# Optimization experiments

Measured on AMD Instinct MI355X. Metric: run time of the kernel, lower is better.

The kernel has to match this reference:

```python
import jax, jax.numpy as jnp
import numpy as np

EPS = 1e-5  # BatchNorm3d default eps


def conv1x1(x, w, b):
    # x: (b, cin, t, h, w); w: (cout, cin); b: (cout,)
    return jnp.einsum('bcthw,oc->bothw', x, w) + b[None, :, None, None, None]


def batchnorm(x):
    # BatchNorm3d(affine=False), training mode: per-channel batch stats over (B,T,H,W)
    mean = jnp.mean(x, axis=(0, 2, 3, 4), keepdims=True)
    var = jnp.var(x, axis=(0, 2, 3, 4), keepdims=True)
    return (x - mean) * jax.lax.rsqrt(var + EPS)


def setup_inputs() -> dict:
    key = jax.random.key(0)
    ks = jax.random.split(key, 9)
    B, C, T, H, W = 4, 512, 16, 14, 14
    IC = C // 4
    s_in = 1.0 / np.sqrt(C)
    s_up = 1.0 / np.sqrt(IC)
    return {
        'maps':    jax.random.normal(ks[0], (B, C, T, H, W), jnp.float32),
        'w_theta': jax.random.uniform(ks[1], (IC, C), jnp.float32, -s_in, s_in),
        'b_theta': jax.random.uniform(ks[2], (IC,),   jnp.float32, -s_in, s_in),
        'w_phalt': jax.random.uniform(ks[3], (IC, C), jnp.float32, -s_in, s_in),
        'b_phalt': jax.random.uniform(ks[4], (IC,),   jnp.float32, -s_in, s_in),
        'w_glob':  jax.random.uniform(ks[5], (IC, C), jnp.float32, -s_in, s_in),
        'b_glob':  jax.random.uniform(ks[6], (IC,),   jnp.float32, -s_in, s_in),
        'w_up':    jax.random.uniform(ks[7], (C, IC), jnp.float32, -s_up, s_up),
        'b_up':    jax.random.uniform(ks[8], (C,),    jnp.float32, -s_up, s_up),
    }


def reference(maps, w_theta, b_theta, w_phalt, b_phalt, w_glob, b_glob, w_up, b_up):
    b, c, t, h, w = maps.shape
    ic = c // 4
    n = t * h * w

    theta_maps = batchnorm(conv1x1(maps, w_theta, b_theta))   # (b, ic, t, h, w)
    phalt_maps = batchnorm(conv1x1(maps, w_phalt, b_phalt))   # computed but UNUSED (bug in original)
    global_maps = batchnorm(conv1x1(maps, w_glob, b_glob))

    theta_x = theta_maps.reshape(b, ic, n)                    # (b, ic, n)
    # NOTE: original code uses theta_maps for phalt_x (faithful to source bug)
    relation = jnp.einsum('bcn,bcm->bnm', theta_x, theta_x)   # (b, n, n)
    relation_normalize = jax.nn.softmax(relation / n, axis=-1)

    global_x = global_maps.reshape(b, ic, n)                  # (b, ic, n)
    y = jnp.einsum('bnm,bcm->bcn', relation_normalize, global_x)
    y = y.reshape(b, ic, t, h, w)

    out = conv1x1(y, w_up, b_up) + maps
    return out
```

## Files before the change

### kernel.cpp

```cpp
#include <hip/hip_runtime.h>
#include <hip/hip_bf16.h>


typedef __attribute__((ext_vector_type(8))) short bf16x8;
typedef __attribute__((ext_vector_type(4))) float f32x4;
typedef __attribute__((ext_vector_type(4))) short s16x4;
typedef __attribute__((ext_vector_type(2))) unsigned int u32x2;

#define NTOK 3136
#define NELEM 1605632
#define NSPLIT 4

__device__ inline float bf2f(short u) {
    union { unsigned int i; float f; } v;
    v.i = ((unsigned int)(unsigned short)u) << 16;
    return v.f;
}
__device__ inline short f2bf(float x) {
    union { float f; unsigned int i; } v;
    v.f = x;
    unsigned int r = v.i + 0x7FFFu + ((v.i >> 16) & 1u);
    return (short)(r >> 16);
}
__device__ inline unsigned int tbf(float x) {
    union { float f; unsigned int i; } v;
    v.f = x;
    return v.i >> 16;
}
__device__ inline void glds16(const void* g, void* l) {
    __builtin_amdgcn_global_load_lds((const __attribute__((address_space(1))) void*)g,
                                     (__attribute__((address_space(3))) void*)l, 16, 0, 0);
}

__global__ __launch_bounds__(256) void prep_w(const float* __restrict__ wt,
                                              const float* __restrict__ wg,
                                              const float* __restrict__ wup,
                                              short* __restrict__ Wb,
                                              short* __restrict__ wupb)
{
    const int i = blockIdx.x * 256 + threadIdx.x;
    if (i < 131072) {
        const int r = i >> 9;
        const int c = i & 511;
        const float w = (r < 128) ? wt[(size_t)r * 512 + c] : wg[(size_t)(r - 128) * 512 + c];
        Wb[i] = f2bf(w);
    } else {
        const int j = i - 131072;
        wupb[j] = f2bf(wup[j]);
    }
}

__global__ __launch_bounds__(256) void conv_in_f(const float* __restrict__ maps,
                                                 const short* __restrict__ Wb,
                                                 short* __restrict__ Tt,
                                                 short* __restrict__ Gpre,
                                                 float* __restrict__ psum,
                                                 float* __restrict__ psq)
{
    const int nt = blockIdx.x, b = blockIdx.y;
    const int n0 = nt * 32;
    const int t = threadIdx.x;
    const int w = __builtin_amdgcn_readfirstlane(t >> 6);
    const int lane = t & 63;
    const int l15 = lane & 15, lhi = lane >> 4;

    __shared__ short Bt[32][136];

    const float* mp = maps + (size_t)b * 512 * NTOK + n0;
    const int cl = t >> 3;
    const int f4 = t & 7;

    f32x4 acc[4][2];
#pragma unroll
    for (int g = 0; g < 4; g++)
#pragma unroll
        for (int j = 0; j < 2; j++) acc[g][j] = f32x4{0.f, 0.f, 0.f, 0.f};

    f32x4 rg[4];
#pragma unroll
    for (int p = 0; p < 4; p++)
        rg[p] = *(const f32x4*)(mp + (size_t)(p * 32 + cl) * NTOK + f4 * 4);

    for (int kc = 0; kc < 4; kc++) {
        __syncthreads();
#pragma unroll
        for (int p = 0; p < 4; p++) {
            const int cc = p * 32 + cl;
#pragma unroll
            for (int i = 0; i < 4; i++) Bt[f4 * 4 + i][cc] = f2bf(rg[p][i]);
        }
        if (kc < 3) {
#pragma unroll
            for (int p = 0; p < 4; p++)
                rg[p] = *(const f32x4*)(mp + (size_t)((kc + 1) * 128 + p * 32 + cl) * NTOK + f4 * 4);
        }
        __syncthreads();
#pragma unroll
        for (int ks = 0; ks < 4; ks++) {
            bf16x8 af[4], bv[2];
#pragma unroll
            for (int g = 0; g < 4; g++)
                af[g] = *(const bf16x8*)(Wb + (size_t)(w * 64 + g * 16 + l15) * 512 + kc * 128 + ks * 32 + lhi * 8);
#pragma unroll
            for (int j = 0; j < 2; j++)
                bv[j] = *(const bf16x8*)(&Bt[j * 16 + l15][ks * 32 + lhi * 8]);
#pragma unroll
            for (int g = 0; g < 4; g++)
#pragma unroll
                for (int j = 0; j < 2; j++)
                    acc[g][j] = __builtin_amdgcn_mfma_f32_16x16x32_bf16(af[g], bv[j], acc[g][j], 0, 0, 0);
        }
    }

    if (w < 2) {
#pragma unroll
        for (int g = 0; g < 4; g++)
#pragma unroll
            for (int j = 0; j < 2; j++) {
                s16x4 v;
#pragma unroll
                for (int r = 0; r < 4; r++) v[r] = f2bf(acc[g][j][r]);
                *(s16x4*)(Tt + ((size_t)b * NTOK + n0 + j * 16 + l15) * 128 + w * 64 + g * 16 + lhi * 4) = v;
            }
    } else {
#pragma unroll
        for (int g = 0; g < 4; g++)
#pragma unroll
            for (int j = 0; j < 2; j++)
#pragma unroll
                for (int r = 0; r < 4; r++) {
                    const int icg = (w - 2) * 64 + g * 16 + lhi * 4 + r;
                    Gpre[((size_t)b * 128 + icg) * NTOK + n0 + j * 16 + l15] = f2bf(acc[g][j][r]);
                }
    }
#pragma unroll
    for (int g = 0; g < 4; g++)
#pragma unroll
        for (int r = 0; r < 4; r++) {
            float s = acc[g][0][r] + acc[g][1][r];
            float q = acc[g][0][r] * acc[g][0][r] + acc[g][1][r] * acc[g][1][r];
#pragma unroll
            for (int off = 1; off < 16; off <<= 1) {
                s += __shfl_xor(s, off);
                q += __shfl_xor(q, off);
            }
            if (l15 == 0) {
                const int ch = w * 64 + g * 16 + lhi * 4 + r;
                psum[(size_t)ch * 392 + b * 98 + nt] = s;
                psq [(size_t)ch * 392 + b * 98 + nt] = q;
            }
        }
}

__global__ __launch_bounds__(64) void stats_fin(const float* __restrict__ psum,
                                                const float* __restrict__ psq,
                                                float* __restrict__ st)
{
    const int ch = blockIdx.x;
    const int lane = threadIdx.x;
    float s = 0.f, q = 0.f;
    for (int i = lane; i < 392; i += 64) {
        s += psum[(size_t)ch * 392 + i];
        q += psq [(size_t)ch * 392 + i];
    }
#pragma unroll
    for (int off = 32; off; off >>= 1) { s += __shfl_xor(s, off); q += __shfl_xor(q, off); }
    if (lane == 0) {
        const float mean = s / 12544.f;
        const float var = q / 12544.f - mean * mean;
        st[ch] = mean;
        st[256 + ch] = rsqrtf(var + 1e-5f);
    }
}

__global__ __launch_bounds__(256) void attn_k(const short* __restrict__ Tt,
                                              const short* __restrict__ Gpre,
                                              const float* __restrict__ st,
                                              float* __restrict__ Opart,
                                              float* __restrict__ dpart)
{
    constexpr int N = NTOK;
    const int b = blockIdx.y, s = blockIdx.z;
    const int w = __builtin_amdgcn_readfirstlane(threadIdx.x >> 6);
    const int lane = threadIdx.x & 63;
    const int l15 = lane & 15, lhi = lane >> 4;
    const int q0w = blockIdx.x * 128 + w * 32;

    __shared__ __align__(16) short Kl[2][64][128];
    __shared__ __align__(16) short Vl[2][128][64];
    __shared__ __align__(16) short Pl[4][32][64];

    const short* tb = Tt + (size_t)b * N * 128;
    const short* gb = Gpre + (size_t)b * 128 * N;

    bf16x8 qf[2][4];
#pragma unroll
    for (int qs = 0; qs < 2; qs++) {
        int row = q0w + qs * 16 + l15;
        row = row < N ? row : N - 1;
#pragma unroll
        for (int ks = 0; ks < 4; ks++) {
            const bf16x8 v = *(const bf16x8*)(tb + (size_t)row * 128 + ks * 32 + lhi * 8);
            const int c0 = ks * 32 + lhi * 8;
            const f32x4 mA = *(const f32x4*)(st + c0);
            const f32x4 mB = *(const f32x4*)(st + c0 + 4);
            const f32x4 rA = *(const f32x4*)(st + 256 + c0);
            const f32x4 rB = *(const f32x4*)(st + 256 + c0 + 4);
            bf16x8 q;
#pragma unroll
            for (int j = 0; j < 4; j++) q[j] = f2bf((bf2f(v[j]) - mA[j]) * (rA[j] * rA[j]));
#pragma unroll
            for (int j = 0; j < 4; j++) q[4 + j] = f2bf((bf2f(v[4 + j]) - mB[j]) * (rB[j] * rB[j]));
            qf[qs][ks] = q;
        }
    }

    f32x4 acc[2][8];
#pragma unroll
    for (int qs = 0; qs < 2; qs++)
#pragma unroll
        for (int is = 0; is < 8; is++) acc[qs][is] = f32x4{0.f, 0.f, 0.f, 0.f};
    float denom[2] = {0.f, 0.f};
    const float inv_n = 1.0f / (float)N;

    auto STAGE = [&](int bufi, int m0) {
#pragma unroll
        for (int i = 0; i < 4; i++) {
            const int rb = w * 16 + i * 4;
            const int krow = rb + (lane >> 4);
            const int ksw = ((lane & 15) * 16) ^ ((krow & 7) << 4);
            glds16((const char*)tb + (size_t)(m0 + krow) * 256 + ksw, (char*)&Kl[bufi][rb][0]);
        }
#pragma unroll
        for (int i = 0; i < 4; i++) {
            const int rb = w * 32 + i * 8;
            const int vrow = rb + (lane >> 3);
            const int vsw = ((lane & 7) * 16) ^ ((vrow & 7) << 4);
            glds16((const char*)gb + ((size_t)vrow * N + m0) * 2 + vsw, (char*)&Vl[bufi][rb][0]);
        }
    };

    const int nt = (49 - s + NSPLIT - 1) / NSPLIT;
    int mt = s;
    STAGE(0, mt * 64);
    __syncthreads();
    int buf = 0;

    const int fK = (l15 & 7) << 4;

    for (int t = 0; t < nt; ++t) {
        if (t + 1 < nt) STAGE(buf ^ 1, (mt + NSPLIT) * 64);

        f32x4 sv[2][4];
#pragma unroll
        for (int qs = 0; qs < 2; qs++)
#pragma unroll
            for (int ms = 0; ms < 4; ms++) sv[qs][ms] = f32x4{0.f, 0.f, 0.f, 0.f};
#pragma unroll
        for (int ms = 0; ms < 4; ms++) {
            const char* kbase = (const char*)&Kl[buf][ms * 16 + l15][0];
#pragma unroll
            for (int ks = 0; ks < 4; ks++) {
                bf16x8 kf = *(const bf16x8*)(kbase + ((ks * 64 + lhi * 16) ^ fK));
                sv[0][ms] = __builtin_amdgcn_mfma_f32_16x16x32_bf16(kf, qf[0][ks], sv[0][ms], 0, 0, 0);
                sv[1][ms] = __builtin_amdgcn_mfma_f32_16x16x32_bf16(kf, qf[1][ks], sv[1][ms], 0, 0, 0);
            }
        }
#pragma unroll
        for (int qs = 0; qs < 2; qs++) {
            char* pbase = (char*)&Pl[w][qs * 16 + l15][0];
#pragma unroll
            for (int ms = 0; ms < 4; ms++) {
                const float p0 = __expf(sv[qs][ms][0] * inv_n);
                const float p1 = __expf(sv[qs][ms][1] * inv_n);
                const float p2 = __expf(sv[qs][ms][2] * inv_n);
                const float p3 = __expf(sv[qs][ms][3] * inv_n);
                denom[qs] += (p0 + p1) + (p2 + p3);
                u32x2 u;
                u[0] = tbf(p0) | (tbf(p1) << 16);
                u[1] = tbf(p2) | (tbf(p3) << 16);
                *(u32x2*)(pbase + ((ms * 32 + lhi * 8) ^ fK)) = u;
            }
        }
#pragma unroll
        for (int kp = 0; kp < 2; kp++) {
            const int coff = kp * 64 + lhi * 16;
            bf16x8 pa[2];
#pragma unroll
            for (int qs = 0; qs < 2; qs++)
                pa[qs] = *(const bf16x8*)((const char*)&Pl[w][qs * 16 + l15][0] + (coff ^ fK));
#pragma unroll
            for (int is = 0; is < 8; is++) {
                bf16x8 vf = *(const bf16x8*)((const char*)&Vl[buf][is * 16 + l15][0] + (coff ^ fK));
                acc[0][is] = __builtin_amdgcn_mfma_f32_16x16x32_bf16(pa[0], vf, acc[0][is], 0, 0, 0);
                acc[1][is] = __builtin_amdgcn_mfma_f32_16x16x32_bf16(pa[1], vf, acc[1][is], 0, 0, 0);
            }
        }
        __syncthreads();
        buf ^= 1;
        mt += NSPLIT;
    }

#pragma unroll
    for (int qs = 0; qs < 2; qs++) {
        denom[qs] += __shfl_xor(denom[qs], 16);
        denom[qs] += __shfl_xor(denom[qs], 32);
    }

    float* op = Opart + ((size_t)(s * 4 + b)) * N * 128;
#pragma unroll
    for (int qs = 0; qs < 2; qs++)
#pragma unroll
        for (int is = 0; is < 8; is++)
#pragma unroll
            for (int r = 0; r < 4; r++) {
                const int n = q0w + qs * 16 + lhi * 4 + r;
                if (n < N) op[(size_t)n * 128 + is * 16 + l15] = acc[qs][is][r];
            }
    if (lhi == 0) {
#pragma unroll
        for (int qs = 0; qs < 2; qs++) {
            const int n = q0w + qs * 16 + l15;
            if (n < N) dpart[(size_t)(s * 4 + b) * N + n] = denom[qs];
        }
    }
}

__global__ __launch_bounds__(256) void conv_out_f(const float* __restrict__ Opart,
                                                  const float* __restrict__ dpart,
                                                  const float* __restrict__ st,
                                                  const short* __restrict__ wupb,
                                                  const float* __restrict__ bup,
                                                  const float* __restrict__ maps,
                                                  float* __restrict__ out)
{
    const int n0 = blockIdx.x * 32, b = blockIdx.y;
    const int t = threadIdx.x;

    __shared__ float denl[32];
    __shared__ __align__(16) short Yl[32][128];

    if (t < 32) {
        float d = 0.f;
#pragma unroll
        for (int s = 0; s < NSPLIT; s++) d += dpart[(size_t)(s * 4 + b) * NTOK + n0 + t];
        denl[t] = 1.0f / d;
    }
    __syncthreads();

#pragma unroll
    for (int g = 0; g < 2; g++) {
        const int e = t + g * 256;
        const int nl = e >> 4, icg = (e & 15) * 8;
        const float rdn = denl[nl];
        float sum[8] = {0.f, 0.f, 0.f, 0.f, 0.f, 0.f, 0.f, 0.f};
#pragma unroll
        for (int s = 0; s < NSPLIT; s++) {
            const size_t base = ((size_t)(s * 4 + b) * NTOK + n0 + nl) * 128 + icg;
            const f32x4 a = *(const f32x4*)(Opart + base);
            const f32x4 c = *(const f32x4*)(Opart + base + 4);
#pragma unroll
            for (int j = 0; j < 4; j++) { sum[j] += a[j]; sum[4 + j] += c[j]; }
        }
        const f32x4 mA = *(const f32x4*)(st + 128 + icg);
        const f32x4 mB = *(const f32x4*)(st + 128 + icg + 4);
        const f32x4 rA = *(const f32x4*)(st + 384 + icg);
        const f32x4 rB = *(const f32x4*)(st + 384 + icg + 4);
        s16x4 v0, v1;
#pragma unroll
        for (int j = 0; j < 4; j++) v0[j] = f2bf((sum[j] * rdn - mA[j]) * rA[j]);
#pragma unroll
        for (int j = 0; j < 4; j++) v1[j] = f2bf((sum[4 + j] * rdn - mB[j]) * rB[j]);
        char* ybase = (char*)&Yl[nl][0];
        const int sw = (nl & 7) << 4;
        *(s16x4*)(ybase + ((icg * 2) ^ sw)) = v0;
        *(s16x4*)(ybase + (((icg * 2) ^ sw) + 8)) = v1;
    }
    __syncthreads();

    const int wv = __builtin_amdgcn_readfirstlane(t >> 6);
    const int lane = t & 63;
    const int l15 = lane & 15, lhi = lane >> 4;
    const int c0 = wv * 128;
    const int fY = (l15 & 7) << 4;

    f32x4 acc[8][2];
#pragma unroll
    for (int g = 0; g < 8; g++)
#pragma unroll
        for (int j = 0; j < 2; j++) acc[g][j] = f32x4{0.f, 0.f, 0.f, 0.f};

#pragma unroll
    for (int ks = 0; ks < 4; ks++) {
        bf16x8 af[8], bv[2];
#pragma unroll
        for (int g = 0; g < 8; g++)
            af[g] = *(const bf16x8*)(wupb + (size_t)(c0 + g * 16 + l15) * 128 + ks * 32 + lhi * 8);
#pragma unroll
        for (int j = 0; j < 2; j++)
            bv[j] = *(const bf16x8*)((const char*)&Yl[j * 16 + l15][0] + ((ks * 64 + lhi * 16) ^ fY));
#pragma unroll
        for (int g = 0; g < 8; g++)
#pragma unroll
            for (int j = 0; j < 2; j++)
                acc[g][j] = __builtin_amdgcn_mfma_f32_16x16x32_bf16(af[g], bv[j], acc[g][j], 0, 0, 0);
    }
#pragma unroll
    for (int g = 0; g < 8; g++)
#pragma unroll
        for (int j = 0; j < 2; j++)
#pragma unroll
            for (int r = 0; r < 4; r++) {
                const int c = c0 + g * 16 + lhi * 4 + r;
                const int n = n0 + j * 16 + l15;
                const size_t o = ((size_t)b * 512 + c) * NTOK + n;
                out[o] = acc[g][j][r] + bup[c] + maps[o];
            }
}

extern "C" void kernel_launch(void* const* d_in, const int* in_sizes, int n_in,
                              void* d_out, int out_size, void* d_ws, size_t ws_size,
                              hipStream_t stream)
{
    const float* maps    = (const float*)d_in[0];
    const float* w_theta = (const float*)d_in[1];
    const float* w_glob  = (const float*)d_in[5];
    const float* w_up    = (const float*)d_in[7];
    const float* b_up    = (const float*)d_in[8];
    float* out = (float*)d_out;

    short* Tt    = (short*)d_ws;
    short* Gpre  = Tt + NELEM;
    short* Wb    = Gpre + NELEM;
    short* wupb  = Wb + 131072;
    float* st    = (float*)(wupb + 65536);
    float* psum  = st + 512;
    float* psq   = psum + 100352;
    float* dpart = psq + 100352;
    float* Opart = dpart + 50176;

    prep_w    <<<768,             256, 0, stream>>>(w_theta, w_glob, w_up, Wb, wupb);
    conv_in_f <<<dim3(98, 4),     256, 0, stream>>>(maps, Wb, Tt, Gpre, psum, psq);
    stats_fin <<<256,             64,  0, stream>>>(psum, psq, st);
    attn_k    <<<dim3(25, 4, NSPLIT), 256, 0, stream>>>(Tt, Gpre, st, Opart, dpart);
    conv_out_f<<<dim3(98, 4),     256, 0, stream>>>(Opart, dpart, st, wupb, b_up, maps, out);
}
```

Measured before the change: 91.88 us.

## Switch attention to 32x32x16 MFMA and keep P in registers via permlane swap

The attention kernel moves from 16x16x32 to 32x32x16 bf16 MFMA tiles for both QK^T and PV. The softmax probabilities are now packed and rearranged in registers with v_permlane32_swap instead of going through a per-wave LDS buffer, which removes the P LDS round-trip and its shared memory. Launch bounds now request 2 blocks per CU. The larger accumulators raise register pressure, and the new fragment mapping must match the 32x32 MFMA layout to stay correct.

```diff
diff --git a/kernel.cpp b/kernel.cpp
--- a/kernel.cpp
+++ b/kernel.cpp
@@ -4,8 +4,8 @@
 
 typedef __attribute__((ext_vector_type(8))) short bf16x8;
 typedef __attribute__((ext_vector_type(4))) float f32x4;
+typedef __attribute__((ext_vector_type(16))) float f32x16;
 typedef __attribute__((ext_vector_type(4))) short s16x4;
-typedef __attribute__((ext_vector_type(2))) unsigned int u32x2;
 
 #define NTOK 3136
 #define NELEM 1605632
@@ -22,10 +22,13 @@
     unsigned int r = v.i + 0x7FFFu + ((v.i >> 16) & 1u);
     return (short)(r >> 16);
 }
-__device__ inline unsigned int tbf(float x) {
-    union { float f; unsigned int i; } v;
-    v.f = x;
-    return v.i >> 16;
+__device__ inline unsigned pk2(float lo, float hi) {
+    union { float f; unsigned u; } a, b;
+    a.f = lo; b.f = hi;
+    return __builtin_amdgcn_perm(b.u, a.u, 0x07060302u);
+}
+__device__ inline void pl32swap(unsigned &a, unsigned &b) {
+    asm("v_permlane32_swap_b32 %0, %1" : "+v"(a), "+v"(b));
 }
 __device__ inline void glds16(const void* g, void* l) {
     __builtin_amdgcn_global_load_lds((const __attribute__((address_space(1))) void*)g,
@@ -173,35 +176,33 @@
     }
 }
 
-__global__ __launch_bounds__(256) void attn_k(const short* __restrict__ Tt,
-                                              const short* __restrict__ Gpre,
-                                              const float* __restrict__ st,
-                                              float* __restrict__ Opart,
-                                              float* __restrict__ dpart)
+__global__ __launch_bounds__(256, 2) void attn_k(const short* __restrict__ Tt,
+                                                 const short* __restrict__ Gpre,
+                                                 const float* __restrict__ st,
+                                                 float* __restrict__ Opart,
+                                                 float* __restrict__ dpart)
 {
     constexpr int N = NTOK;
     const int b = blockIdx.y, s = blockIdx.z;
     const int w = __builtin_amdgcn_readfirstlane(threadIdx.x >> 6);
     const int lane = threadIdx.x & 63;
-    const int l15 = lane & 15, lhi = lane >> 4;
+    const int l31 = lane & 31, hi = lane >> 5;
     const int q0w = blockIdx.x * 128 + w * 32;
 
     __shared__ __align__(16) short Kl[2][64][128];
     __shared__ __align__(16) short Vl[2][128][64];
-    __shared__ __align__(16) short Pl[4][32][64];
 
     const short* tb = Tt + (size_t)b * N * 128;
     const short* gb = Gpre + (size_t)b * 128 * N;
 
-    bf16x8 qf[2][4];
-#pragma unroll
-    for (int qs = 0; qs < 2; qs++) {
-        int row = q0w + qs * 16 + l15;
-        row = row < N ? row : N - 1;
-#pragma unroll
-        for (int ks = 0; ks < 4; ks++) {
-            const bf16x8 v = *(const bf16x8*)(tb + (size_t)row * 128 + ks * 32 + lhi * 8);
-            const int c0 = ks * 32 + lhi * 8;
+    bf16x8 qf[8];
+    {
+        int row = q0w + l31; row = row < N ? row : N - 1;
+        const short* qp = tb + (size_t)row * 128;
+#pragma unroll
+        for (int ks = 0; ks < 8; ks++) {
+            const int c0 = ks * 16 + hi * 8;
+            const bf16x8 v = *(const bf16x8*)(qp + c0);
             const f32x4 mA = *(const f32x4*)(st + c0);
             const f32x4 mB = *(const f32x4*)(st + c0 + 4);
             const f32x4 rA = *(const f32x4*)(st + 256 + c0);
@@ -211,16 +212,16 @@
             for (int j = 0; j < 4; j++) q[j] = f2bf((bf2f(v[j]) - mA[j]) * (rA[j] * rA[j]));
 #pragma unroll
             for (int j = 0; j < 4; j++) q[4 + j] = f2bf((bf2f(v[4 + j]) - mB[j]) * (rB[j] * rB[j]));
-            qf[qs][ks] = q;
-        }
-    }
-
-    f32x4 acc[2][8];
-#pragma unroll
-    for (int qs = 0; qs < 2; qs++)
-#pragma unroll
-        for (int is = 0; is < 8; is++) acc[qs][is] = f32x4{0.f, 0.f, 0.f, 0.f};
-    float denom[2] = {0.f, 0.f};
+            qf[ks] = q;
+        }
+    }
+
+    f32x16 accv[4];
+#pragma unroll
+    for (int it = 0; it < 4; it++)
+#pragma unroll
+        for (int r = 0; r < 16; r++) accv[it][r] = 0.f;
+    float denom = 0.f;
     const float inv_n = 1.0f / (float)N;
 
     auto STAGE = [&](int bufi, int m0) {
@@ -228,15 +229,15 @@
         for (int i = 0; i < 4; i++) {
             const int rb = w * 16 + i * 4;
             const int krow = rb + (lane >> 4);
-            const int ksw = ((lane & 15) * 16) ^ ((krow & 7) << 4);
-            glds16((const char*)tb + (size_t)(m0 + krow) * 256 + ksw, (char*)&Kl[bufi][rb][0]);
+            const int ls = (lane & 15) ^ (krow & 7);
+            glds16(tb + (size_t)(m0 + krow) * 128 + ls * 8, (void*)&Kl[bufi][rb][0]);
         }
 #pragma unroll
         for (int i = 0; i < 4; i++) {
             const int rb = w * 32 + i * 8;
             const int vrow = rb + (lane >> 3);
-            const int vsw = ((lane & 7) * 16) ^ ((vrow & 7) << 4);
-            glds16((const char*)gb + ((size_t)vrow * N + m0) * 2 + vsw, (char*)&Vl[bufi][rb][0]);
+            const int ls = (lane & 7) ^ (vrow & 7);
+            glds16(gb + (size_t)vrow * N + m0 + ls * 8, (void*)&Vl[bufi][rb][0]);
         }
     };
 
@@ -246,54 +247,50 @@
     __syncthreads();
     int buf = 0;
 
-    const int fK = (l15 & 7) << 4;
+    const int fr = (l31 & 7) << 4;
+
+    auto mkpa = [&](const f32x16 &sv, bf16x8 *dst) {
+        float e[16];
+#pragma unroll
+        for (int r = 0; r < 16; r++) { e[r] = __expf(sv[r] * inv_n); denom += e[r]; }
+        unsigned c0 = pk2(e[0], e[1]),  c1 = pk2(e[2], e[3]);
+        unsigned c2 = pk2(e[4], e[5]),  c3 = pk2(e[6], e[7]);
+        unsigned c4 = pk2(e[8], e[9]),  c5 = pk2(e[10], e[11]);
+        unsigned c6 = pk2(e[12], e[13]), c7 = pk2(e[14], e[15]);
+        pl32swap(c0, c2); pl32swap(c1, c3); pl32swap(c4, c6); pl32swap(c5, c7);
+        union U { unsigned u[4]; bf16x8 v; } f0, f1;
+        f0.u[0] = c0; f0.u[1] = c1; f0.u[2] = c2; f0.u[3] = c3;
+        f1.u[0] = c4; f1.u[1] = c5; f1.u[2] = c6; f1.u[3] = c7;
+        dst[0] = f0.v; dst[1] = f1.v;
+    };
 
     for (int t = 0; t < nt; ++t) {
         if (t + 1 < nt) STAGE(buf ^ 1, (mt + NSPLIT) * 64);
 
-        f32x4 sv[2][4];
-#pragma unroll
-        for (int qs = 0; qs < 2; qs++)
-#pragma unroll
-            for (int ms = 0; ms < 4; ms++) sv[qs][ms] = f32x4{0.f, 0.f, 0.f, 0.f};
-#pragma unroll
-        for (int ms = 0; ms < 4; ms++) {
-            const char* kbase = (const char*)&Kl[buf][ms * 16 + l15][0];
-#pragma unroll
-            for (int ks = 0; ks < 4; ks++) {
-                bf16x8 kf = *(const bf16x8*)(kbase + ((ks * 64 + lhi * 16) ^ fK));
-                sv[0][ms] = __builtin_amdgcn_mfma_f32_16x16x32_bf16(kf, qf[0][ks], sv[0][ms], 0, 0, 0);
-                sv[1][ms] = __builtin_amdgcn_mfma_f32_16x16x32_bf16(kf, qf[1][ks], sv[1][ms], 0, 0, 0);
-            }
-        }
-#pragma unroll
-        for (int qs = 0; qs < 2; qs++) {
-            char* pbase = (char*)&Pl[w][qs * 16 + l15][0];
-#pragma unroll
-            for (int ms = 0; ms < 4; ms++) {
-                const float p0 = __expf(sv[qs][ms][0] * inv_n);
-                const float p1 = __expf(sv[qs][ms][1] * inv_n);
-                const float p2 = __expf(sv[qs][ms][2] * inv_n);
-                const float p3 = __expf(sv[qs][ms][3] * inv_n);
-                denom[qs] += (p0 + p1) + (p2 + p3);
-                u32x2 u;
-                u[0] = tbf(p0) | (tbf(p1) << 16);
-                u[1] = tbf(p2) | (tbf(p3) << 16);
-                *(u32x2*)(pbase + ((ms * 32 + lhi * 8) ^ fK)) = u;
-            }
-        }
-#pragma unroll
-        for (int kp = 0; kp < 2; kp++) {
-            const int coff = kp * 64 + lhi * 16;
-            bf16x8 pa[2];
-#pragma unroll
-            for (int qs = 0; qs < 2; qs++)
-                pa[qs] = *(const bf16x8*)((const char*)&Pl[w][qs * 16 + l15][0] + (coff ^ fK));
-#pragma unroll
-            for (int is = 0; is < 8; is++) {
-                bf16x8 vf = *(const bf16x8*)((const char*)&Vl[buf][is * 16 + l15][0] + (coff ^ fK));
-                acc[0][is] = __builtin_amdgcn_mfma_f32_16x16x32_bf16(pa[0], vf, acc[0][is], 0, 0, 0);
-                acc[1][is] = __builtin_amdgcn_mfma_f32_16x16x32_bf16(pa[1], vf, acc[1][is], 0, 0, 0);
+        f32x16 sv0, sv1;
+#pragma unroll
+        for (int r = 0; r < 16; r++) { sv0[r] = 0.f; sv1[r] = 0.f; }
+#pragma unroll
+        for (int ks = 0; ks < 8; ks++) {
+            const int co = (ks * 32 + hi * 16) ^ fr;
+            bf16x8 kf0 = *(const bf16x8*)((const char*)&Kl[buf][l31][0] + co);
+            bf16x8 kf1 = *(const bf16x8*)((const char*)&Kl[buf][32 + l31][0] + co);
+            sv0 = __builtin_amdgcn_mfma_f32_32x32x16_bf16(kf0, qf[ks], sv0, 0, 0, 0);
+            sv1 = __builtin_amdgcn_mfma_f32_32x32x16_bf16(kf1, qf[ks], sv1, 0, 0, 0);
+        }
+
+        bf16x8 pa[4];
+        mkpa(sv0, &pa[0]);
+        mkpa(sv1, &pa[2]);
+
+#pragma unroll
+        for (int kp = 0; kp < 4; kp++) {
+            const int cv = kp * 32 + hi * 16;
+#pragma unroll
+            for (int it = 0; it < 4; it++) {
+                const int row = it * 32 + l31;
+                bf16x8 vf = *(const bf16x8*)((const char*)&Vl[buf][row][0] + (cv ^ fr));
+                accv[it] = __builtin_amdgcn_mfma_f32_32x32x16_bf16(pa[kp], vf, accv[it], 0, 0, 0);
             }
         }
         __syncthreads();
@@ -301,28 +298,19 @@
         mt += NSPLIT;
     }
 
-#pragma unroll
-    for (int qs = 0; qs < 2; qs++) {
-        denom[qs] += __shfl_xor(denom[qs], 16);
-        denom[qs] += __shfl_xor(denom[qs], 32);
-    }
+    denom += __shfl_xor(denom, 32);
 
     float* op = Opart + ((size_t)(s * 4 + b)) * N * 128;
 #pragma unroll
-    for (int qs = 0; qs < 2; qs++)
-#pragma unroll
-        for (int is = 0; is < 8; is++)
-#pragma unroll
-            for (int r = 0; r < 4; r++) {
-                const int n = q0w + qs * 16 + lhi * 4 + r;
-                if (n < N) op[(size_t)n * 128 + is * 16 + l15] = acc[qs][is][r];
-            }
-    if (lhi == 0) {
-#pragma unroll
-        for (int qs = 0; qs < 2; qs++) {
-            const int n = q0w + qs * 16 + l15;
-            if (n < N) dpart[(size_t)(s * 4 + b) * N + n] = denom[qs];
-        }
+    for (int it = 0; it < 4; it++)
+#pragma unroll
+        for (int r = 0; r < 16; r++) {
+            const int n = q0w + (r & 3) + 8 * (r >> 2) + 4 * hi;
+            if (n < N) op[(size_t)n * 128 + it * 32 + l31] = accv[it][r];
+        }
+    if (lane < 32) {
+        const int n = q0w + l31;
+        if (n < N) dpart[(size_t)(s * 4 + b) * N + n] = denom;
     }
 }
 
```

Measured after the change: 87.53 us. -4.7%, faster.
